# Kernel optimization log

Measured on AMD Instinct MI355X. Metric: run time of the kernel, lower is better.

Reference implementation:

```python
import jax, jax.numpy as jnp
import numpy as np

NUM_USERS = 100000
NUM_ITEMS = 200000
D = 128          # embedding_dim
K = 4            # num interest heads
B = 4096
H = 256          # history length
H1, H2 = 512, 256  # hidden_units


def setup_inputs() -> dict:
    key = jax.random.key(0)
    ks = jax.random.split(key, 10)
    inp = {
        "user_ids": jax.random.randint(ks[0], (B,), 0, NUM_USERS),
        "candidate_items": jax.random.randint(ks[1], (B,), 0, NUM_ITEMS),
        "history_items": jax.random.randint(ks[2], (B, H), 0, NUM_ITEMS),
        "item_table": jax.random.normal(ks[3], (NUM_ITEMS, D), dtype=jnp.float32) * 0.05,
        "Wp": jax.random.normal(ks[4], (D, K), dtype=jnp.float32) * (1.0 / np.sqrt(D)),
        "W1": jax.random.normal(ks[5], (2 * D, H1), dtype=jnp.float32) * (1.0 / np.sqrt(2 * D)),
        "b1": jnp.zeros((H1,), dtype=jnp.float32),
        "W2": jax.random.normal(ks[6], (H1, H2), dtype=jnp.float32) * (1.0 / np.sqrt(H1)),
        "b2": jnp.zeros((H2,), dtype=jnp.float32),
        "W3": jax.random.normal(ks[7], (H2, 1), dtype=jnp.float32) * (1.0 / np.sqrt(H2)),
        "b3": jnp.zeros((1,), dtype=jnp.float32),
    }
    return inp


def reference(user_ids, candidate_items, history_items, item_table, Wp,
              W1, b1, W2, b2, W3, b3):
    # user_ids is unused by the original forward (user_emb never applied)
    item_vecs = item_table[history_items]          # (B, H, D)
    cand_vec = item_table[candidate_items]         # (B, D)

    # per-interest attention scores, softmax over history axis
    scores = jnp.einsum('bhd,dk->bhk', item_vecs, Wp)   # (B, H, K)
    scores = jax.nn.softmax(scores, axis=1)

    # softmax-weighted pooling -> K interest vectors per user
    interest_vectors = jnp.einsum('bhk,bhd->bkd', scores, item_vecs)  # (B, K, D)

    # similarity to candidate, pick best interest (data-dependent gather)
    sim_scores = jnp.einsum('bkd,bd->bk', interest_vectors, cand_vec)  # (B, K)
    best_idx = jnp.argmax(sim_scores, axis=-1)                          # (B,)
    selected = jnp.take_along_axis(
        interest_vectors, best_idx[:, None, None], axis=1)[:, 0, :]    # (B, D)

    # MLP tail: [2D -> 512] ReLU [512 -> 256] ReLU [256 -> 1], sigmoid
    x = jnp.concatenate([selected, cand_vec], axis=-1)  # (B, 2D)
    x = jax.nn.relu(x @ W1 + b1)
    x = jax.nn.relu(x @ W2 + b2)
    out = (x @ W3 + b3)[:, 0]                            # (B,)
    return jax.nn.sigmoid(out)
```

## Files before the change

### kernel.cpp

```cpp
#include <hip/hip_runtime.h>
#include <hip/hip_bf16.h>
#include <math.h>

#define B_SZ   4096
#define H_LEN  256
#define D_DIM  128
#define K_HEADS 4
#define H1_DIM 512
#define H2_DIM 256
#define NUM_ITEMS 200000

#define CH     64
#define NCH    4
#define TPAD   132

typedef __attribute__((ext_vector_type(8))) short bf16x8;
typedef __attribute__((ext_vector_type(4))) float f32x4;

#define LDS_BARRIER() do {                                   \
    asm volatile("s_waitcnt lgkmcnt(0)" ::: "memory");       \
    __builtin_amdgcn_s_barrier();                            \
} while (0)

__device__ __forceinline__ float bf2f(short s) {
    unsigned u = ((unsigned)(unsigned short)s) << 16;
    float f; __builtin_memcpy(&f, &u, 4); return f;
}

__global__ __launch_bounds__(256, 4) void interest_kernel_bf16(
    const int*   __restrict__ cand_ids,
    const int*   __restrict__ hist,
    const float* __restrict__ table,
    const __hip_bfloat16* __restrict__ tableB,
    const float* __restrict__ Wp,
    __hip_bfloat16* __restrict__ Xbf)
{
    __shared__ float tile[CH * TPAD];
    __shared__ float wpt[K_HEADS * D_DIM];
    __shared__ float exps4[CH * 4];
    __shared__ float candv[D_DIM];
    __shared__ int   rowids[H_LEN];
    __shared__ float lsumW[16];
    __shared__ float simred[4][K_HEADS];
    __shared__ int   bestk;

    const int b    = blockIdx.x;
    const int t    = threadIdx.x;
    const int lane = t & 63, w = t >> 6;
    const int r    = t >> 2, q = t & 3;
    const int d    = t & 127, half = t >> 7;

    if (t < D_DIM) {
        float4 w4 = ((const float4*)Wp)[t];
        wpt[0 * D_DIM + t] = w4.x;
        wpt[1 * D_DIM + t] = w4.y;
        wpt[2 * D_DIM + t] = w4.z;
        wpt[3 * D_DIM + t] = w4.w;
    }
    const int cand = cand_ids[b];
    if (t >= 128 && t < 160) {
        int c = t - 128;
        ((float4*)candv)[c] = ((const float4*)(table + (long long)cand * D_DIM))[c];
    }
    rowids[t] = hist[(long long)b * H_LEN + t];

    bf16x8 v0, v1, v2, v3;
    {
        const int row0 = hist[(long long)b * H_LEN + r];
        const __hip_bfloat16* rp = tableB + (long long)row0 * D_DIM + (q << 3);
        v0 = *(const bf16x8*)(rp + 0 * 32);
        v1 = *(const bf16x8*)(rp + 1 * 32);
        v2 = *(const bf16x8*)(rp + 2 * 32);
        v3 = *(const bf16x8*)(rp + 3 * 32);
    }

    LDS_BARRIER();

    float a0 = 0.f, a1 = 0.f, a2 = 0.f, a3 = 0.f;
    float l0 = 0.f, l1 = 0.f, l2 = 0.f, l3 = 0.f;

    for (int c = 0; c < NCH; ++c) {
        bf16x8 u0, u1, u2, u3;
        if (c + 1 < NCH) {
            const int row = rowids[((c + 1) << 6) + r];
            const __hip_bfloat16* rp = tableB + (long long)row * D_DIM + (q << 3);
            u0 = *(const bf16x8*)(rp + 0 * 32);
            u1 = *(const bf16x8*)(rp + 1 * 32);
            u2 = *(const bf16x8*)(rp + 2 * 32);
            u3 = *(const bf16x8*)(rp + 3 * 32);
        }

        float s0 = 0.f, s1 = 0.f, s2 = 0.f, s3 = 0.f;
        #define DO_J(JJ, VV)                                                    \
        {   const int cb = (q << 3) + (JJ << 5);                                \
            float f0 = bf2f(VV[0]), f1 = bf2f(VV[1]);                           \
            float f2 = bf2f(VV[2]), f3 = bf2f(VV[3]);                           \
            float f4 = bf2f(VV[4]), f5 = bf2f(VV[5]);                           \
            float f6 = bf2f(VV[6]), f7 = bf2f(VV[7]);                           \
            float4 wA, wB;                                                      \
            wA = *(const float4*)(wpt + 0 * D_DIM + cb);                        \
            wB = *(const float4*)(wpt + 0 * D_DIM + cb + 4);                    \
            s0 += f0*wA.x + f1*wA.y + f2*wA.z + f3*wA.w                         \
                + f4*wB.x + f5*wB.y + f6*wB.z + f7*wB.w;                        \
            wA = *(const float4*)(wpt + 1 * D_DIM + cb);                        \
            wB = *(const float4*)(wpt + 1 * D_DIM + cb + 4);                    \
            s1 += f0*wA.x + f1*wA.y + f2*wA.z + f3*wA.w                         \
                + f4*wB.x + f5*wB.y + f6*wB.z + f7*wB.w;                        \
            wA = *(const float4*)(wpt + 2 * D_DIM + cb);                        \
            wB = *(const float4*)(wpt + 2 * D_DIM + cb + 4);                    \
            s2 += f0*wA.x + f1*wA.y + f2*wA.z + f3*wA.w                         \
                + f4*wB.x + f5*wB.y + f6*wB.z + f7*wB.w;                        \
            wA = *(const float4*)(wpt + 3 * D_DIM + cb);                        \
            wB = *(const float4*)(wpt + 3 * D_DIM + cb + 4);                    \
            s3 += f0*wA.x + f1*wA.y + f2*wA.z + f3*wA.w                         \
                + f4*wB.x + f5*wB.y + f6*wB.z + f7*wB.w;                        \
            *(float4*)(tile + r * TPAD + cb)     = make_float4(f0, f1, f2, f3); \
            *(float4*)(tile + r * TPAD + cb + 4) = make_float4(f4, f5, f6, f7); \
        }
        DO_J(0, v0) DO_J(1, v1) DO_J(2, v2) DO_J(3, v3)
        #undef DO_J

        s0 += __shfl_xor(s0, 1); s0 += __shfl_xor(s0, 2);
        s1 += __shfl_xor(s1, 1); s1 += __shfl_xor(s1, 2);
        s2 += __shfl_xor(s2, 1); s2 += __shfl_xor(s2, 2);
        s3 += __shfl_xor(s3, 1); s3 += __shfl_xor(s3, 2);

        float e0 = expf(s0), e1 = expf(s1), e2 = expf(s2), e3 = expf(s3);
        if (q == 0) ((float4*)exps4)[r] = make_float4(e0, e1, e2, e3);

        float t0 = e0, t1 = e1, t2 = e2, t3 = e3;
        #pragma unroll
        for (int off = 4; off <= 32; off <<= 1) {
            t0 += __shfl_xor(t0, off);
            t1 += __shfl_xor(t1, off);
            t2 += __shfl_xor(t2, off);
            t3 += __shfl_xor(t3, off);
        }
        l0 += t0; l1 += t1; l2 += t2; l3 += t3;

        LDS_BARRIER();

        #pragma unroll 8
        for (int i = 0; i < 32; ++i) {
            int hl = (half << 5) + i;
            float4 e4 = ((const float4*)exps4)[hl];
            float  vv = tile[hl * TPAD + d];
            a0 += e4.x * vv; a1 += e4.y * vv; a2 += e4.z * vv; a3 += e4.w * vv;
        }

        LDS_BARRIER();

        if (c + 1 < NCH) { v0 = u0; v1 = u1; v2 = u2; v3 = u3; }
    }

    __syncthreads();
    float* partBp = tile;
    float* ivbufp = tile + 512;

    if (half == 1) ((float4*)partBp)[d] = make_float4(a0, a1, a2, a3);
    if (lane == 0) ((float4*)lsumW)[w]  = make_float4(l0, l1, l2, l3);
    __syncthreads();

    float s0 = 0.f, s1 = 0.f, s2 = 0.f, s3 = 0.f;
    if (half == 0) {
        float4 pb = ((const float4*)partBp)[d];
        float4 L0 = ((const float4*)lsumW)[0];
        float4 L1 = ((const float4*)lsumW)[1];
        float4 L2 = ((const float4*)lsumW)[2];
        float4 L3 = ((const float4*)lsumW)[3];
        float i0 = 1.f / (L0.x + L1.x + L2.x + L3.x);
        float i1 = 1.f / (L0.y + L1.y + L2.y + L3.y);
        float i2 = 1.f / (L0.z + L1.z + L2.z + L3.z);
        float i3 = 1.f / (L0.w + L1.w + L2.w + L3.w);
        a0 = (a0 + pb.x) * i0;
        a1 = (a1 + pb.y) * i1;
        a2 = (a2 + pb.z) * i2;
        a3 = (a3 + pb.w) * i3;
        ((float4*)ivbufp)[d] = make_float4(a0, a1, a2, a3);
        float cd = candv[d];
        s0 = a0 * cd; s1 = a1 * cd; s2 = a2 * cd; s3 = a3 * cd;
    }
    #pragma unroll
    for (int off = 32; off >= 1; off >>= 1) {
        s0 += __shfl_xor(s0, off);
        s1 += __shfl_xor(s1, off);
        s2 += __shfl_xor(s2, off);
        s3 += __shfl_xor(s3, off);
    }
    if (lane == 0) {
        simred[w][0] = s0; simred[w][1] = s1;
        simred[w][2] = s2; simred[w][3] = s3;
    }
    __syncthreads();

    if (t == 0) {
        float sim[4];
        #pragma unroll
        for (int k = 0; k < 4; ++k)
            sim[k] = simred[0][k] + simred[1][k] + simred[2][k] + simred[3][k];
        int best = 0;
        #pragma unroll
        for (int k = 1; k < 4; ++k) if (sim[k] > sim[best]) best = k;
        bestk = best;
    }
    __syncthreads();

    __hip_bfloat16* xrow = Xbf + (long long)b * (2 * D_DIM);
    if (t < 128) xrow[t] = __float2bfloat16(ivbufp[t * 4 + bestk]);
    else         xrow[t] = __float2bfloat16(candv[t - 128]);
}

__global__ __launch_bounds__(256, 6) void interest_kernel_f32(
    const int*   __restrict__ cand_ids, const int* __restrict__ hist,
    const float* __restrict__ table, const float* __restrict__ Wp,
    __hip_bfloat16* __restrict__ Xbf)
{
    __shared__ float tile[32 * TPAD];
    __shared__ float wpt[K_HEADS * D_DIM];
    __shared__ float exps4[32 * 4];
    __shared__ float candv[D_DIM];
    __shared__ int   rowids[H_LEN];
    __shared__ float lsumW[16];
    __shared__ float simred[4][K_HEADS];
    __shared__ int   bestk;

    const int b    = blockIdx.x;
    const int t    = threadIdx.x;
    const int lane = t & 63, w = t >> 6;
    const int r    = t >> 3, q = t & 7;
    const int d    = t & 127, half = t >> 7;

    if (t < D_DIM) {
        float4 w4 = ((const float4*)Wp)[t];
        wpt[0 * D_DIM + t] = w4.x; wpt[1 * D_DIM + t] = w4.y;
        wpt[2 * D_DIM + t] = w4.z; wpt[3 * D_DIM + t] = w4.w;
    }
    const int cand = cand_ids[b];
    if (t >= 128 && t < 160) {
        int c = t - 128;
        ((float4*)candv)[c] = ((const float4*)(table + (long long)cand * D_DIM))[c];
    }
    rowids[t] = hist[(long long)b * H_LEN + t];

    float4 v0, v1, v2, v3;
    {
        const int row0 = hist[(long long)b * H_LEN + r];
        const float* rp = table + (long long)row0 * D_DIM + (q << 2);
        v0 = *(const float4*)(rp + 0 * 32); v1 = *(const float4*)(rp + 1 * 32);
        v2 = *(const float4*)(rp + 2 * 32); v3 = *(const float4*)(rp + 3 * 32);
    }
    LDS_BARRIER();

    float a0 = 0.f, a1 = 0.f, a2 = 0.f, a3 = 0.f;
    float l0 = 0.f, l1 = 0.f, l2 = 0.f, l3 = 0.f;

    for (int c = 0; c < 8; ++c) {
        float4 u0, u1, u2, u3;
        if (c + 1 < 8) {
            const int row = rowids[((c + 1) << 5) + r];
            const float* rp = table + (long long)row * D_DIM + (q << 2);
            u0 = *(const float4*)(rp + 0 * 32); u1 = *(const float4*)(rp + 1 * 32);
            u2 = *(const float4*)(rp + 2 * 32); u3 = *(const float4*)(rp + 3 * 32);
        }
        float s0 = 0.f, s1 = 0.f, s2 = 0.f, s3 = 0.f;
        float4 va;
        #define DO_J(JJ, VV)                                                    \
        {   va = VV;                                                            \
            const int cb = (q << 2) + (JJ << 5);                                \
            float4 w0 = *(const float4*)(wpt + 0 * D_DIM + cb);                 \
            float4 w1 = *(const float4*)(wpt + 1 * D_DIM + cb);                 \
            float4 w2 = *(const float4*)(wpt + 2 * D_DIM + cb);                 \
            float4 w3 = *(const float4*)(wpt + 3 * D_DIM + cb);                 \
            s0 += va.x*w0.x + va.y*w0.y + va.z*w0.z + va.w*w0.w;                \
            s1 += va.x*w1.x + va.y*w1.y + va.z*w1.z + va.w*w1.w;                \
            s2 += va.x*w2.x + va.y*w2.y + va.z*w2.z + va.w*w2.w;                \
            s3 += va.x*w3.x + va.y*w3.y + va.z*w3.z + va.w*w3.w;                \
            *(float4*)(tile + r * TPAD + cb) = va;                              \
        }
        DO_J(0, v0) DO_J(1, v1) DO_J(2, v2) DO_J(3, v3)
        #undef DO_J

        s0 += __shfl_xor(s0, 1); s0 += __shfl_xor(s0, 2); s0 += __shfl_xor(s0, 4);
        s1 += __shfl_xor(s1, 1); s1 += __shfl_xor(s1, 2); s1 += __shfl_xor(s1, 4);
        s2 += __shfl_xor(s2, 1); s2 += __shfl_xor(s2, 2); s2 += __shfl_xor(s2, 4);
        s3 += __shfl_xor(s3, 1); s3 += __shfl_xor(s3, 2); s3 += __shfl_xor(s3, 4);

        float e0 = expf(s0), e1 = expf(s1), e2 = expf(s2), e3 = expf(s3);
        if (q == 0) ((float4*)exps4)[r] = make_float4(e0, e1, e2, e3);

        float t0 = e0, t1 = e1, t2 = e2, t3 = e3;
        #pragma unroll
        for (int off = 8; off <= 32; off <<= 1) {
            t0 += __shfl_xor(t0, off); t1 += __shfl_xor(t1, off);
            t2 += __shfl_xor(t2, off); t3 += __shfl_xor(t3, off);
        }
        l0 += t0; l1 += t1; l2 += t2; l3 += t3;

        LDS_BARRIER();
        #pragma unroll
        for (int i = 0; i < 16; ++i) {
            int hl = (half << 4) + i;
            float4 e4 = ((const float4*)exps4)[hl];
            float  vv = tile[hl * TPAD + d];
            a0 += e4.x * vv; a1 += e4.y * vv; a2 += e4.z * vv; a3 += e4.w * vv;
        }
        LDS_BARRIER();
        if (c + 1 < 8) { v0 = u0; v1 = u1; v2 = u2; v3 = u3; }
    }

    __syncthreads();
    float* partBp = tile;
    float* ivbufp = tile + 512;

    if (half == 1) ((float4*)partBp)[d] = make_float4(a0, a1, a2, a3);
    if (lane == 0) ((float4*)lsumW)[w]  = make_float4(l0, l1, l2, l3);
    __syncthreads();

    float s0 = 0.f, s1 = 0.f, s2 = 0.f, s3 = 0.f;
    if (half == 0) {
        float4 pb = ((const float4*)partBp)[d];
        float4 L0 = ((const float4*)lsumW)[0];
        float4 L1 = ((const float4*)lsumW)[1];
        float4 L2 = ((const float4*)lsumW)[2];
        float4 L3 = ((const float4*)lsumW)[3];
        float i0 = 1.f / (L0.x + L1.x + L2.x + L3.x);
        float i1 = 1.f / (L0.y + L1.y + L2.y + L3.y);
        float i2 = 1.f / (L0.z + L1.z + L2.z + L3.z);
        float i3 = 1.f / (L0.w + L1.w + L2.w + L3.w);
        a0 = (a0 + pb.x) * i0; a1 = (a1 + pb.y) * i1;
        a2 = (a2 + pb.z) * i2; a3 = (a3 + pb.w) * i3;
        ((float4*)ivbufp)[d] = make_float4(a0, a1, a2, a3);
        float cd = candv[d];
        s0 = a0 * cd; s1 = a1 * cd; s2 = a2 * cd; s3 = a3 * cd;
    }
    #pragma unroll
    for (int off = 32; off >= 1; off >>= 1) {
        s0 += __shfl_xor(s0, off); s1 += __shfl_xor(s1, off);
        s2 += __shfl_xor(s2, off); s3 += __shfl_xor(s3, off);
    }
    if (lane == 0) {
        simred[w][0] = s0; simred[w][1] = s1;
        simred[w][2] = s2; simred[w][3] = s3;
    }
    __syncthreads();
    if (t == 0) {
        float sim[4];
        #pragma unroll
        for (int k = 0; k < 4; ++k)
            sim[k] = simred[0][k] + simred[1][k] + simred[2][k] + simred[3][k];
        int best = 0;
        #pragma unroll
        for (int k = 1; k < 4; ++k) if (sim[k] > sim[best]) best = k;
        bestk = best;
    }
    __syncthreads();

    __hip_bfloat16* xrow = Xbf + (long long)b * (2 * D_DIM);
    if (t < 128) xrow[t] = __float2bfloat16(ivbufp[t * 4 + bestk]);
    else         xrow[t] = __float2bfloat16(candv[t - 128]);
}

__global__ __launch_bounds__(256) void convert_all(
    const float* __restrict__ table,
    const float* __restrict__ W1, const float* __restrict__ W2,
    __hip_bfloat16* __restrict__ tableB,
    __hip_bfloat16* __restrict__ W1t, __hip_bfloat16* __restrict__ W2t)
{
    __shared__ float tl[32][33];
    int bid = blockIdx.x;
    if (bid < 12500) {
        long long idx = (long long)bid * 256 + threadIdx.x;
        const float4* s = (const float4*)table + idx * 2;
        float4 s0 = s[0], s1 = s[1];
        __hip_bfloat16 o[8];
        o[0] = __float2bfloat16(s0.x); o[1] = __float2bfloat16(s0.y);
        o[2] = __float2bfloat16(s0.z); o[3] = __float2bfloat16(s0.w);
        o[4] = __float2bfloat16(s1.x); o[5] = __float2bfloat16(s1.y);
        o[6] = __float2bfloat16(s1.z); o[7] = __float2bfloat16(s1.w);
        *(uint4*)(tableB + idx * 8) = *(uint4*)o;
        return;
    }
    bid -= 12500;
    const float* W; __hip_bfloat16* Wt; int K, N;
    if (bid < 128) { W = W1; Wt = W1t; K = 2 * D_DIM; N = H1_DIM; }
    else           { W = W2; Wt = W2t; K = H1_DIM;    N = H2_DIM; bid -= 128; }
    const int ntn = N >> 5;
    const int k0 = (bid / ntn) << 5, n0 = (bid % ntn) << 5;
    const int tx = threadIdx.x & 31, ty = threadIdx.x >> 5;
    #pragma unroll
    for (int j = 0; j < 4; ++j)
        tl[ty + 8 * j][tx] = W[(long long)(k0 + ty + 8 * j) * N + n0 + tx];
    __syncthreads();
    #pragma unroll
    for (int j = 0; j < 4; ++j)
        Wt[(long long)(n0 + ty + 8 * j) * K + k0 + tx] =
            __float2bfloat16(tl[tx][ty + 8 * j]);
}

__global__ __launch_bounds__(256) void convert_weights(
    const float* __restrict__ W1, const float* __restrict__ W2,
    __hip_bfloat16* __restrict__ W1t, __hip_bfloat16* __restrict__ W2t)
{
    __shared__ float tl[32][33];
    int bid = blockIdx.x;
    const float* W; __hip_bfloat16* Wt; int K, N;
    if (bid < 128) { W = W1; Wt = W1t; K = 2 * D_DIM; N = H1_DIM; }
    else           { W = W2; Wt = W2t; K = H1_DIM;    N = H2_DIM; bid -= 128; }
    const int ntn = N >> 5;
    const int k0 = (bid / ntn) << 5, n0 = (bid % ntn) << 5;
    const int tx = threadIdx.x & 31, ty = threadIdx.x >> 5;
    #pragma unroll
    for (int j = 0; j < 4; ++j)
        tl[ty + 8 * j][tx] = W[(long long)(k0 + ty + 8 * j) * N + n0 + tx];
    __syncthreads();
    #pragma unroll
    for (int j = 0; j < 4; ++j)
        Wt[(long long)(n0 + ty + 8 * j) * K + k0 + tx] =
            __float2bfloat16(tl[tx][ty + 8 * j]);
}

__global__ __launch_bounds__(1024) void mlp_fused(
    const __hip_bfloat16* __restrict__ X,
    const __hip_bfloat16* __restrict__ W1t,
    const float* __restrict__ b1,
    const __hip_bfloat16* __restrict__ W2t,
    const float* __restrict__ b2,
    const float* __restrict__ W3,
    const float* __restrict__ b3,
    float*       __restrict__ out)
{
    __shared__ __hip_bfloat16 h1[16][H1_DIM + 8];
    __shared__ float          h2[16][H2_DIM + 4];

    const int t    = threadIdx.x;
    const int wave = t >> 6, lane = t & 63;
    const int lm   = lane & 15, quad = lane >> 4;
    const int m0   = blockIdx.x * 16;

    const __hip_bfloat16* Ap = X + (long long)(m0 + lm) * (2 * D_DIM) + quad * 8;
    bf16x8 af[8];
    #pragma unroll
    for (int it = 0; it < 8; ++it) af[it] = *(const bf16x8*)(Ap + it * 32);

    #pragma unroll
    for (int tn = 0; tn < 2; ++tn) {
        const int n0 = (wave * 2 + tn) * 16;
        const __hip_bfloat16* Bp = W1t + (long long)(n0 + lm) * (2 * D_DIM) + quad * 8;
        f32x4 acc = {0.f, 0.f, 0.f, 0.f};
        #pragma unroll
        for (int it = 0; it < 8; ++it) {
            bf16x8 bfr = *(const bf16x8*)(Bp + it * 32);
            acc = __builtin_amdgcn_mfma_f32_16x16x32_bf16(af[it], bfr, acc, 0, 0, 0);
        }
        const float bv = b1[n0 + lm];
        #pragma unroll
        for (int i = 0; i < 4; ++i)
            h1[quad * 4 + i][n0 + lm] = __float2bfloat16(fmaxf(acc[i] + bv, 0.f));
    }
    __syncthreads();

    {
        const int n0 = wave * 16;
        const __hip_bfloat16* Bp = W2t + (long long)(n0 + lm) * H1_DIM + quad * 8;
        f32x4 acc = {0.f, 0.f, 0.f, 0.f};
        #pragma unroll
        for (int it = 0; it < 16; ++it) {
            bf16x8 a2  = *(const bf16x8*)(&h1[lm][quad * 8 + it * 32]);
            bf16x8 bfr = *(const bf16x8*)(Bp + it * 32);
            acc = __builtin_amdgcn_mfma_f32_16x16x32_bf16(a2, bfr, acc, 0, 0, 0);
        }
        const float bv = b2[n0 + lm];
        #pragma unroll
        for (int i = 0; i < 4; ++i)
            h2[quad * 4 + i][n0 + lm] = fmaxf(acc[i] + bv, 0.f);
    }
    __syncthreads();

    {
        const int row = wave;
        float4 hv = *(const float4*)(&h2[row][lane * 4]);
        float4 w4 = ((const float4*)W3)[lane];
        float s = hv.x * w4.x + hv.y * w4.y + hv.z * w4.z + hv.w * w4.w;
        #pragma unroll
        for (int off = 1; off <= 32; off <<= 1) s += __shfl_xor(s, off);
        if (lane == 0)
            out[m0 + row] = 1.f / (1.f + expf(-(s + b3[0])));
    }
}

extern "C" void kernel_launch(void* const* d_in, const int* in_sizes, int n_in,
                              void* d_out, int out_size, void* d_ws, size_t ws_size,
                              hipStream_t stream) {
    const int*   cand  = (const int*)  d_in[1];
    const int*   hist  = (const int*)  d_in[2];
    const float* table = (const float*)d_in[3];
    const float* Wp    = (const float*)d_in[4];
    const float* W1    = (const float*)d_in[5];
    const float* b1    = (const float*)d_in[6];
    const float* W2    = (const float*)d_in[7];
    const float* b2    = (const float*)d_in[8];
    const float* W3    = (const float*)d_in[9];
    const float* b3    = (const float*)d_in[10];
    float* out = (float*)d_out;

    char* p = (char*)d_ws;
    __hip_bfloat16* Xbf = (__hip_bfloat16*)p;  p += (size_t)B_SZ * 2 * D_DIM * 2;
    __hip_bfloat16* W1t = (__hip_bfloat16*)p;  p += (size_t)H1_DIM * 2 * D_DIM * 2;
    __hip_bfloat16* W2t = (__hip_bfloat16*)p;  p += (size_t)H1_DIM * H2_DIM * 2;
    __hip_bfloat16* tableB = (__hip_bfloat16*)p;
    const size_t need = ((char*)tableB - (char*)d_ws) + (size_t)NUM_ITEMS * D_DIM * 2;

    if (ws_size >= need) {
        convert_all<<<12500 + 256, 256, 0, stream>>>(table, W1, W2, tableB, W1t, W2t);
        interest_kernel_bf16<<<B_SZ, 256, 0, stream>>>(cand, hist, table, tableB, Wp, Xbf);
    } else {
        convert_weights<<<256, 256, 0, stream>>>(W1, W2, W1t, W2t);
        interest_kernel_f32<<<B_SZ, 256, 0, stream>>>(cand, hist, table, Wp, Xbf);
    }
    mlp_fused<<<B_SZ / 16, 1024, 0, stream>>>(Xbf, W1t, b1, W2t, b2, W3, b3, out);
}
```

Before: 275.7 us.

## Store bf16 history tile in LDS, split pooling across four waves, halve MLP block

The interest kernel now keeps the staged history chunk in LDS as bf16 instead of fp32. This halves shared memory per block and allows a higher occupancy hint (6 blocks per CU). The pooling loop is redistributed so each wave handles 16 rows and each thread two adjacent dims, and the cross-wave reduction and argmax are folded into a single wave, dropping one barrier. Separately, the MLP kernel now uses 512 threads: each wave computes more output tiles and reuses layer-2 A fragments held in registers, at the cost of more register pressure.

Result: slower. 548.9 us (+99.1%).

```diff
diff --git a/kernel.cpp b/kernel.cpp
--- a/kernel.cpp
+++ b/kernel.cpp
@@ -12,6 +12,7 @@
 
 #define CH     64
 #define NCH    4
+#define TP2    136
 #define TPAD   132
 
 typedef __attribute__((ext_vector_type(8))) short bf16x8;
@@ -27,7 +28,7 @@
     float f; __builtin_memcpy(&f, &u, 4); return f;
 }
 
-__global__ __launch_bounds__(256, 4) void interest_kernel_bf16(
+__global__ __launch_bounds__(256, 6) void interest_kernel_bf16(
     const int*   __restrict__ cand_ids,
     const int*   __restrict__ hist,
     const float* __restrict__ table,
@@ -35,20 +36,19 @@
     const float* __restrict__ Wp,
     __hip_bfloat16* __restrict__ Xbf)
 {
-    __shared__ float tile[CH * TPAD];
+    __shared__ __align__(16) short tileB[CH * TP2];
     __shared__ float wpt[K_HEADS * D_DIM];
     __shared__ float exps4[CH * 4];
     __shared__ float candv[D_DIM];
     __shared__ int   rowids[H_LEN];
     __shared__ float lsumW[16];
-    __shared__ float simred[4][K_HEADS];
     __shared__ int   bestk;
 
     const int b    = blockIdx.x;
     const int t    = threadIdx.x;
     const int lane = t & 63, w = t >> 6;
     const int r    = t >> 2, q = t & 3;
-    const int d    = t & 127, half = t >> 7;
+    const int d2   = t & 63;
 
     if (t < D_DIM) {
         float4 w4 = ((const float4*)Wp)[t];
@@ -76,7 +76,8 @@
 
     LDS_BARRIER();
 
-    float a0 = 0.f, a1 = 0.f, a2 = 0.f, a3 = 0.f;
+    float a0x = 0.f, a0y = 0.f, a1x = 0.f, a1y = 0.f;
+    float a2x = 0.f, a2y = 0.f, a3x = 0.f, a3y = 0.f;
     float l0 = 0.f, l1 = 0.f, l2 = 0.f, l3 = 0.f;
 
     for (int c = 0; c < NCH; ++c) {
@@ -114,8 +115,7 @@
             wB = *(const float4*)(wpt + 3 * D_DIM + cb + 4);                    \
             s3 += f0*wA.x + f1*wA.y + f2*wA.z + f3*wA.w                         \
                 + f4*wB.x + f5*wB.y + f6*wB.z + f7*wB.w;                        \
-            *(float4*)(tile + r * TPAD + cb)     = make_float4(f0, f1, f2, f3); \
-            *(float4*)(tile + r * TPAD + cb + 4) = make_float4(f4, f5, f6, f7); \
+            *(bf16x8*)(tileB + r * TP2 + cb) = VV;                              \
         }
         DO_J(0, v0) DO_J(1, v1) DO_J(2, v2) DO_J(3, v3)
         #undef DO_J
@@ -140,12 +140,17 @@
 
         LDS_BARRIER();
 
-        #pragma unroll 8
-        for (int i = 0; i < 32; ++i) {
-            int hl = (half << 5) + i;
+        #pragma unroll
+        for (int i = 0; i < 16; ++i) {
+            const int hl = (w << 4) + i;
             float4 e4 = ((const float4*)exps4)[hl];
-            float  vv = tile[hl * TPAD + d];
-            a0 += e4.x * vv; a1 += e4.y * vv; a2 += e4.z * vv; a3 += e4.w * vv;
+            unsigned pv = *(const unsigned*)(tileB + hl * TP2 + (d2 << 1));
+            float fe = bf2f((short)(pv & 0xffff));
+            float fo = bf2f((short)(pv >> 16));
+            a0x += e4.x * fe; a0y += e4.x * fo;
+            a1x += e4.y * fe; a1y += e4.y * fo;
+            a2x += e4.z * fe; a2y += e4.z * fo;
+            a3x += e4.w * fe; a3y += e4.w * fo;
         }
 
         LDS_BARRIER();
@@ -154,16 +159,25 @@
     }
 
     __syncthreads();
-    float* partBp = tile;
-    float* ivbufp = tile + 512;
-
-    if (half == 1) ((float4*)partBp)[d] = make_float4(a0, a1, a2, a3);
-    if (lane == 0) ((float4*)lsumW)[w]  = make_float4(l0, l1, l2, l3);
-    __syncthreads();
-
-    float s0 = 0.f, s1 = 0.f, s2 = 0.f, s3 = 0.f;
-    if (half == 0) {
-        float4 pb = ((const float4*)partBp)[d];
+    float* scratch = (float*)tileB;
+    float* ivbufp  = scratch + 1536;
+
+    if (w) {
+        float4* sp = (float4*)(scratch + (((w - 1) << 6) + d2) * 8);
+        sp[0] = make_float4(a0x, a0y, a1x, a1y);
+        sp[1] = make_float4(a2x, a2y, a3x, a3y);
+    }
+    if (lane == 0) ((float4*)lsumW)[w] = make_float4(l0, l1, l2, l3);
+    __syncthreads();
+
+    if (w == 0) {
+        #pragma unroll
+        for (int gg = 0; gg < 3; ++gg) {
+            const float4* sp = (const float4*)(scratch + ((gg << 6) + d2) * 8);
+            float4 p0 = sp[0], p1 = sp[1];
+            a0x += p0.x; a0y += p0.y; a1x += p0.z; a1y += p0.w;
+            a2x += p1.x; a2y += p1.y; a3x += p1.z; a3y += p1.w;
+        }
         float4 L0 = ((const float4*)lsumW)[0];
         float4 L1 = ((const float4*)lsumW)[1];
         float4 L2 = ((const float4*)lsumW)[2];
@@ -172,36 +186,29 @@
         float i1 = 1.f / (L0.y + L1.y + L2.y + L3.y);
         float i2 = 1.f / (L0.z + L1.z + L2.z + L3.z);
         float i3 = 1.f / (L0.w + L1.w + L2.w + L3.w);
-        a0 = (a0 + pb.x) * i0;
-        a1 = (a1 + pb.y) * i1;
-        a2 = (a2 + pb.z) * i2;
-        a3 = (a3 + pb.w) * i3;
-        ((float4*)ivbufp)[d] = make_float4(a0, a1, a2, a3);
-        float cd = candv[d];
-        s0 = a0 * cd; s1 = a1 * cd; s2 = a2 * cd; s3 = a3 * cd;
-    }
-    #pragma unroll
-    for (int off = 32; off >= 1; off >>= 1) {
-        s0 += __shfl_xor(s0, off);
-        s1 += __shfl_xor(s1, off);
-        s2 += __shfl_xor(s2, off);
-        s3 += __shfl_xor(s3, off);
-    }
-    if (lane == 0) {
-        simred[w][0] = s0; simred[w][1] = s1;
-        simred[w][2] = s2; simred[w][3] = s3;
-    }
-    __syncthreads();
-
-    if (t == 0) {
-        float sim[4];
-        #pragma unroll
-        for (int k = 0; k < 4; ++k)
-            sim[k] = simred[0][k] + simred[1][k] + simred[2][k] + simred[3][k];
-        int best = 0;
-        #pragma unroll
-        for (int k = 1; k < 4; ++k) if (sim[k] > sim[best]) best = k;
-        bestk = best;
+        a0x *= i0; a0y *= i0; a1x *= i1; a1y *= i1;
+        a2x *= i2; a2y *= i2; a3x *= i3; a3y *= i3;
+        ((float4*)ivbufp)[d2 * 2 + 0] = make_float4(a0x, a1x, a2x, a3x);
+        ((float4*)ivbufp)[d2 * 2 + 1] = make_float4(a0y, a1y, a2y, a3y);
+        float c0 = candv[d2 * 2], c1 = candv[d2 * 2 + 1];
+        float s0 = a0x * c0 + a0y * c1;
+        float s1 = a1x * c0 + a1y * c1;
+        float s2 = a2x * c0 + a2y * c1;
+        float s3 = a3x * c0 + a3y * c1;
+        #pragma unroll
+        for (int off = 1; off <= 32; off <<= 1) {
+            s0 += __shfl_xor(s0, off);
+            s1 += __shfl_xor(s1, off);
+            s2 += __shfl_xor(s2, off);
+            s3 += __shfl_xor(s3, off);
+        }
+        if (t == 0) {
+            float sim[4] = {s0, s1, s2, s3};
+            int best = 0;
+            #pragma unroll
+            for (int k = 1; k < 4; ++k) if (sim[k] > sim[best]) best = k;
+            bestk = best;
+        }
     }
     __syncthreads();
 
@@ -419,7 +426,7 @@
             __float2bfloat16(tl[tx][ty + 8 * j]);
 }
 
-__global__ __launch_bounds__(1024) void mlp_fused(
+__global__ __launch_bounds__(512) void mlp_fused(
     const __hip_bfloat16* __restrict__ X,
     const __hip_bfloat16* __restrict__ W1t,
     const float* __restrict__ b1,
@@ -443,8 +450,8 @@
     for (int it = 0; it < 8; ++it) af[it] = *(const bf16x8*)(Ap + it * 32);
 
     #pragma unroll
-    for (int tn = 0; tn < 2; ++tn) {
-        const int n0 = (wave * 2 + tn) * 16;
+    for (int tn = 0; tn < 4; ++tn) {
+        const int n0 = (wave * 4 + tn) * 16;
         const __hip_bfloat16* Bp = W1t + (long long)(n0 + lm) * (2 * D_DIM) + quad * 8;
         f32x4 acc = {0.f, 0.f, 0.f, 0.f};
         #pragma unroll
@@ -459,15 +466,20 @@
     }
     __syncthreads();
 
-    {
-        const int n0 = wave * 16;
+    bf16x8 a2[16];
+    #pragma unroll
+    for (int it = 0; it < 16; ++it)
+        a2[it] = *(const bf16x8*)(&h1[lm][quad * 8 + it * 32]);
+
+    #pragma unroll
+    for (int tn = 0; tn < 2; ++tn) {
+        const int n0 = (wave * 2 + tn) * 16;
         const __hip_bfloat16* Bp = W2t + (long long)(n0 + lm) * H1_DIM + quad * 8;
         f32x4 acc = {0.f, 0.f, 0.f, 0.f};
         #pragma unroll
         for (int it = 0; it < 16; ++it) {
-            bf16x8 a2  = *(const bf16x8*)(&h1[lm][quad * 8 + it * 32]);
             bf16x8 bfr = *(const bf16x8*)(Bp + it * 32);
-            acc = __builtin_amdgcn_mfma_f32_16x16x32_bf16(a2, bfr, acc, 0, 0, 0);
+            acc = __builtin_amdgcn_mfma_f32_16x16x32_bf16(a2[it], bfr, acc, 0, 0, 0);
         }
         const float bv = b2[n0 + lm];
         #pragma unroll
@@ -477,13 +489,13 @@
     __syncthreads();
 
     {
-        const int row = wave;
-        float4 hv = *(const float4*)(&h2[row][lane * 4]);
-        float4 w4 = ((const float4*)W3)[lane];
-        float s = hv.x * w4.x + hv.y * w4.y + hv.z * w4.z + hv.w * w4.w;
-        #pragma unroll
-        for (int off = 1; off <= 32; off <<= 1) s += __shfl_xor(s, off);
-        if (lane == 0)
+        const int row = t >> 5, c = (t & 31) * 8;
+        float s = 0.f;
+        #pragma unroll
+        for (int j = 0; j < 8; ++j) s += h2[row][c + j] * W3[c + j];
+        #pragma unroll
+        for (int off = 1; off <= 16; off <<= 1) s += __shfl_xor(s, off);
+        if ((lane & 31) == 0)
             out[m0 + row] = 1.f / (1.f + expf(-(s + b3[0])));
     }
 }
@@ -517,5 +529,5 @@
         convert_weights<<<256, 256, 0, stream>>>(W1, W2, W1t, W2t);
         interest_kernel_f32<<<B_SZ, 256, 0, stream>>>(cand, hist, table, Wp, Xbf);
     }
-    mlp_fused<<<B_SZ / 16, 1024, 0, stream>>>(Xbf, W1t, b1, W2t, b2, W3, b3, out);
-}
+    mlp_fused<<<B_SZ / 16, 512, 0, stream>>>(Xbf, W1t, b1, W2t, b2, W3, b3, out);
+}
```
